# Optimization experiments

Measured on AMD Instinct MI355X. Metric: run time of the kernel, lower is better.

## Reference

```python
import jax, jax.numpy as jnp
import numpy as np

B, S, H, I, E, K = 4, 2048, 1024, 4096, 8, 2


def setup_inputs() -> dict:
    key = jax.random.key(0)
    ks = jax.random.split(key, 5)
    scale = 1.0 / np.sqrt(H)
    return {
        "hidden_states": jax.random.normal(ks[0], (B, S, H), dtype=jnp.float32),
        "router_w": jax.random.normal(ks[1], (E, H), dtype=jnp.float32) * scale,
        "gate_w": jax.random.normal(ks[2], (E, I, H), dtype=jnp.float32) * scale,
        "up_w": jax.random.normal(ks[3], (E, I, H), dtype=jnp.float32) * scale,
        "down_w": jax.random.normal(ks[4], (E, H, I), dtype=jnp.float32) * (1.0 / np.sqrt(I)),
        "top_k": K,
    }


def reference(hidden_states, router_w, gate_w, up_w, down_w, top_k):
    # Router: logits -> softmax -> top-k -> renormalized weights (eval mode, no jitter)
    logits = jnp.einsum("bsh,eh->bse", hidden_states, router_w)
    probs = jax.nn.softmax(logits, axis=-1)
    expert_weights, expert_indices = jax.lax.top_k(probs, top_k)  # [B,S,K]
    expert_weights = expert_weights / expert_weights.sum(axis=-1, keepdims=True)

    n_experts = router_w.shape[0]
    # Per-token combine weight for each expert: [B,S,E]
    combine = (jax.nn.one_hot(expert_indices, n_experts, dtype=expert_weights.dtype)
               * expert_weights[..., None]).sum(axis=-2)

    out = jnp.zeros_like(hidden_states)
    for e in range(n_experts):  # fixed small expert count
        g = jax.nn.silu(hidden_states @ gate_w[e].T)  # [B,S,I]
        u = hidden_states @ up_w[e].T                 # [B,S,I]
        y = (g * u) @ down_w[e].T                     # [B,S,H]
        out = out + combine[..., e:e + 1] * y
    return out
```

## Files before the change

### kernel.cpp

```cpp
#include <hip/hip_runtime.h>
#include <hip/hip_bf16.h>
#include <math.h>
#include <stdint.h>

#define TOKENS 8192
#define HD 1024
#define ID 4096
#define NE 8
#define RMAX 18432
#define MAXT 72

typedef __attribute__((ext_vector_type(8))) short short8v;
typedef __attribute__((ext_vector_type(4))) float f32x4;

typedef const __attribute__((address_space(1))) unsigned int* gas_u32p;
typedef __attribute__((address_space(3))) unsigned int* las_u32p;

__device__ __forceinline__ void stage16(const void* g, void* l) {
  __builtin_amdgcn_global_load_lds((gas_u32p)g, (las_u32p)l, 16, 0, 0);
}

#define BARRIER asm volatile("s_barrier" ::: "memory")
#define WAITLGKM asm volatile("s_waitcnt lgkmcnt(0)" ::: "memory")
#define VMC0 asm volatile("s_waitcnt vmcnt(0)" ::: "memory")
#define VMC3 asm volatile("s_waitcnt vmcnt(3)" ::: "memory")
#define VMC6 asm volatile("s_waitcnt vmcnt(6)" ::: "memory")

__global__ __launch_bounds__(256) void convert_kernel(const float* __restrict__ src,
                                                      __hip_bfloat16* __restrict__ dst) {
  size_t i = ((size_t)blockIdx.x * 256 + threadIdx.x) * 8;
  float4 a = ((const float4*)(src + i))[0];
  float4 b = ((const float4*)(src + i))[1];
  union { __hip_bfloat16 h[8]; int4 v; } u;
  u.h[0] = __float2bfloat16(a.x); u.h[1] = __float2bfloat16(a.y);
  u.h[2] = __float2bfloat16(a.z); u.h[3] = __float2bfloat16(a.w);
  u.h[4] = __float2bfloat16(b.x); u.h[5] = __float2bfloat16(b.y);
  u.h[6] = __float2bfloat16(b.z); u.h[7] = __float2bfloat16(b.w);
  *(int4*)(dst + i) = u.v;
}

__global__ __launch_bounds__(256) void router_kernel(
    const float* __restrict__ h, const float* __restrict__ rw,
    __hip_bfloat16* __restrict__ hx, int* __restrict__ tidx,
    float* __restrict__ tw, int* __restrict__ cnt) {
  int wid = threadIdx.x >> 6, lane = threadIdx.x & 63;
  int t = blockIdx.x * 4 + wid;
  const float4* h4 = (const float4*)(h + (size_t)t * HD);
  float x[16];
  {
    float4 xa = h4[lane * 4 + 0], xb = h4[lane * 4 + 1], xc = h4[lane * 4 + 2], xd = h4[lane * 4 + 3];
    x[0] = xa.x; x[1] = xa.y; x[2] = xa.z; x[3] = xa.w;
    x[4] = xb.x; x[5] = xb.y; x[6] = xb.z; x[7] = xb.w;
    x[8] = xc.x; x[9] = xc.y; x[10] = xc.z; x[11] = xc.w;
    x[12] = xd.x; x[13] = xd.y; x[14] = xd.z; x[15] = xd.w;
  }
  union { __hip_bfloat16 hb[16]; int4 v[2]; } u;
#pragma unroll
  for (int j = 0; j < 16; j++) u.hb[j] = __float2bfloat16(x[j]);
  {
    int4* hxp = (int4*)(hx + (size_t)t * HD + lane * 16);
    hxp[0] = u.v[0]; hxp[1] = u.v[1];
  }
  double acc[NE];
#pragma unroll
  for (int e = 0; e < NE; e++) {
    const float4* w4 = (const float4*)(rw + e * HD);
    float4 wa = w4[lane * 4 + 0], wb = w4[lane * 4 + 1], wc = w4[lane * 4 + 2], wd = w4[lane * 4 + 3];
    double s = 0.0;
    s += (double)x[0] * wa.x + (double)x[1] * wa.y + (double)x[2] * wa.z + (double)x[3] * wa.w;
    s += (double)x[4] * wb.x + (double)x[5] * wb.y + (double)x[6] * wb.z + (double)x[7] * wb.w;
    s += (double)x[8] * wc.x + (double)x[9] * wc.y + (double)x[10] * wc.z + (double)x[11] * wc.w;
    s += (double)x[12] * wd.x + (double)x[13] * wd.y + (double)x[14] * wd.z + (double)x[15] * wd.w;
    acc[e] = s;
  }
#pragma unroll
  for (int off = 32; off >= 1; off >>= 1)
#pragma unroll
    for (int e = 0; e < NE; e++) acc[e] += __shfl_xor(acc[e], off, 64);
  if (lane == 0) {
    int i0 = 0; double l0 = acc[0];
#pragma unroll
    for (int e = 1; e < NE; e++) if (acc[e] > l0) { l0 = acc[e]; i0 = e; }
    int i1 = -1; double l1 = -1.0e300;
#pragma unroll
    for (int e = 0; e < NE; e++) if (e != i0 && acc[e] > l1) { l1 = acc[e]; i1 = e; }
    double r = exp(l1 - l0);
    float w0 = (float)(1.0 / (1.0 + r));
    float w1 = (float)(r / (1.0 + r));
    tidx[t * 2 + 0] = i0; tidx[t * 2 + 1] = i1;
    tw[t * 2 + 0] = w0;  tw[t * 2 + 1] = w1;
    atomicAdd(&cnt[i0], 1); atomicAdd(&cnt[i1], 1);
  }
}

__global__ void scan_kernel(const int* __restrict__ cnt, int* __restrict__ ofs, int* __restrict__ cnt2) {
  if (threadIdx.x == 0) {
    int a = 0;
    for (int e = 0; e < NE; e++) { ofs[e] = a; a += (cnt[e] + 255) & ~255; }
    ofs[NE] = a;
  }
  if (threadIdx.x < NE) cnt2[threadIdx.x] = 0;
}

__global__ __launch_bounds__(256) void scatter_kernel(
    const int* __restrict__ tidx, const float* __restrict__ tw,
    const int* __restrict__ ofs, int* __restrict__ cnt2,
    int* __restrict__ rowmap, int* __restrict__ slots) {
  int t = blockIdx.x * 256 + threadIdx.x;
#pragma unroll
  for (int k = 0; k < 2; k++) {
    int e = tidx[t * 2 + k];
    int pos = atomicAdd(&cnt2[e], 1);
    int row = ofs[e] + pos;
    rowmap[row] = t;
    slots[t * 2 + k] = row;
  }
}

#define MFMAQ(ACC, MO, NO, AF, BF)                                                         \
  { _Pragma("unroll") for (int m_ = 0; m_ < 4; m_++)                                       \
    _Pragma("unroll") for (int n_ = 0; n_ < 2; n_++)                                       \
    _Pragma("unroll") for (int k_ = 0; k_ < 2; k_++)                                       \
      ACC[(MO) + m_][(NO) + n_] = __builtin_amdgcn_mfma_f32_16x16x32_bf16(                 \
          AF[m_][k_], BF[n_][k_], ACC[(MO) + m_][(NO) + n_], 0, 0, 0); }

__global__ __launch_bounds__(512, 2) void gemm1_kernel(
    const __hip_bfloat16* __restrict__ hx, const __hip_bfloat16* __restrict__ Wg,
    const __hip_bfloat16* __restrict__ Wu, const int* __restrict__ rowmap,
    const int* __restrict__ ofs, const __hip_bfloat16* __restrict__ zrow,
    __hip_bfloat16* __restrict__ act) {
  __shared__ __align__(128) char lds[131072];
  const int nwg = gridDim.x;
  int wg0 = blockIdx.x;
  int wg = (wg0 & 7) * (nwg >> 3) + (wg0 >> 3);
  const int tm = wg >> 5, tn = wg & 31;
  const int Rtot = ofs[NE];
  const int row0 = tm * 256;
  if (row0 >= Rtot) return;
  int e = 0;
#pragma unroll
  for (int i = 1; i < NE; i++) e += (row0 >= ofs[i]);
  const int tid = threadIdx.x, wid = tid >> 6, lane = tid & 63;
  const int wm = wid >> 1, wn = wid & 1;
  const int fr = lane & 15, fkE = (lane >> 4) << 3;
  const int wmB = wm * 64, wnB = wn * 64;

  const char* srcA[4]; const char* srcG[2]; const char* srcU[2];
  int ldA[4], ldG[2], ldU[2];
#pragma unroll
  for (int j = 0; j < 4; j++) {
    int d = j * 8192 + tid * 16;
    int row = d >> 7;
    int kb = (d ^ (((d >> 7) & 7) << 4)) & 127;
    int tok = rowmap[row0 + row];
    const __hip_bfloat16* base = (tok >= 0) ? (hx + (size_t)tok * HD) : zrow;
    srcA[j] = (const char*)base + kb;
    ldA[j] = j * 8192 + wid * 1024;
  }
#pragma unroll
  for (int j = 0; j < 2; j++) {
    int d = j * 8192 + tid * 16;
    int row = d >> 7;
    int kb = (d ^ (((d >> 7) & 7) << 4)) & 127;
    srcG[j] = (const char*)(Wg + ((size_t)e * ID + tn * 128 + row) * HD) + kb;
    srcU[j] = (const char*)(Wu + ((size_t)e * ID + tn * 128 + row) * HD) + kb;
    ldG[j] = 32768 + j * 8192 + wid * 1024;
    ldU[j] = 49152 + j * 8192 + wid * 1024;
  }
#define STG_A(j, t, bf) stage16(srcA[j] + (size_t)(t) * 128, (char*)lds + (bf) * 65536 + ldA[j])
#define STG_G(j, t, bf) stage16(srcG[j] + (size_t)(t) * 128, (char*)lds + (bf) * 65536 + ldG[j])
#define STG_U(j, t, bf) stage16(srcU[j] + (size_t)(t) * 128, (char*)lds + (bf) * 65536 + ldU[j])

  auto RD = [&](int bf, int poff, int rowi, int kki) -> short8v {
    int o = ((rowi + fr) << 7) + ((kki << 5) + fkE) * 2;
    o ^= ((o >> 7) & 7) << 4;
    return *(const short8v*)(&lds[bf * 65536 + poff + o]);
  };

  f32x4 accG[4][4], accU[4][4];
#pragma unroll
  for (int m = 0; m < 4; m++)
#pragma unroll
    for (int n = 0; n < 4; n++) { accG[m][n] = (f32x4)(0.0f); accU[m][n] = (f32x4)(0.0f); }

  const int NT = HD / 64;
#pragma unroll
  for (int j = 0; j < 4; j++) STG_A(j, 0, 0);
#pragma unroll
  for (int j = 0; j < 2; j++) STG_G(j, 0, 0);
#pragma unroll
  for (int j = 0; j < 2; j++) STG_U(j, 0, 0);
#pragma unroll
  for (int j = 0; j < 4; j++) STG_A(j, 1, 1);
#pragma unroll
  for (int j = 0; j < 2; j++) STG_G(j, 1, 1);
  VMC6; BARRIER;

#pragma unroll 1
  for (int I = 0; I < NT / 2; ++I) {
    const int t0 = 2 * I;
    const bool more = (t0 + 2 < NT);
    short8v a[4][2], bA[2][2], bB[2][2];
#pragma unroll
    for (int m = 0; m < 4; m++) { a[m][0] = RD(0, 0, wmB + m * 16, 0); a[m][1] = RD(0, 0, wmB + m * 16, 1); }
#pragma unroll
    for (int n = 0; n < 2; n++) { bA[n][0] = RD(0, 32768, wnB + n * 16, 0); bA[n][1] = RD(0, 32768, wnB + n * 16, 1); }
    STG_U(0, t0 + 1, 1); STG_U(1, t0 + 1, 1);
    BARRIER; WAITLGKM;
    __builtin_amdgcn_s_setprio(1); MFMAQ(accG, 0, 0, a, bA); __builtin_amdgcn_s_setprio(0);
    BARRIER;
#pragma unroll
    for (int n = 0; n < 2; n++) { bB[n][0] = RD(0, 32768, wnB + 32 + n * 16, 0); bB[n][1] = RD(0, 32768, wnB + 32 + n * 16, 1); }
    if (more) { STG_A(0, t0 + 2, 0); STG_A(1, t0 + 2, 0); }
    BARRIER; WAITLGKM;
    __builtin_amdgcn_s_setprio(1); MFMAQ(accG, 0, 2, a, bB); __builtin_amdgcn_s_setprio(0);
    BARRIER;
#pragma unroll
    for (int n = 0; n < 2; n++) { bA[n][0] = RD(0, 49152, wnB + n * 16, 0); bA[n][1] = RD(0, 49152, wnB + n * 16, 1); }
    if (more) { STG_A(2, t0 + 2, 0); STG_A(3, t0 + 2, 0); }
    BARRIER; WAITLGKM;
    __builtin_amdgcn_s_setprio(1); MFMAQ(accU, 0, 0, a, bA); __builtin_amdgcn_s_setprio(0);
    BARRIER;
#pragma unroll
    for (int n = 0; n < 2; n++) { bB[n][0] = RD(0, 49152, wnB + 32 + n * 16, 0); bB[n][1] = RD(0, 49152, wnB + 32 + n * 16, 1); }
    if (more) { STG_G(0, t0 + 2, 0); STG_G(1, t0 + 2, 0); }
    BARRIER; WAITLGKM;
    __builtin_amdgcn_s_setprio(1); MFMAQ(accU, 0, 2, a, bB); __builtin_amdgcn_s_setprio(0);
    if (more) { VMC6; } else { VMC0; }
    BARRIER;
#pragma unroll
    for (int m = 0; m < 4; m++) { a[m][0] = RD(1, 0, wmB + m * 16, 0); a[m][1] = RD(1, 0, wmB + m * 16, 1); }
#pragma unroll
    for (int n = 0; n < 2; n++) { bA[n][0] = RD(1, 32768, wnB + n * 16, 0); bA[n][1] = RD(1, 32768, wnB + n * 16, 1); }
    if (more) { STG_U(0, t0 + 2, 0); STG_U(1, t0 + 2, 0); }
    BARRIER; WAITLGKM;
    __builtin_amdgcn_s_setprio(1); MFMAQ(accG, 0, 0, a, bA); __builtin_amdgcn_s_setprio(0);
    BARRIER;
#pragma unroll
    for (int n = 0; n < 2; n++) { bB[n][0] = RD(1, 32768, wnB + 32 + n * 16, 0); bB[n][1] = RD(1, 32768, wnB + 32 + n * 16, 1); }
    if (more) { STG_A(0, t0 + 3, 1); STG_A(1, t0 + 3, 1); }
    BARRIER; WAITLGKM;
    __builtin_amdgcn_s_setprio(1); MFMAQ(accG, 0, 2, a, bB); __builtin_amdgcn_s_setprio(0);
    BARRIER;
#pragma unroll
    for (int n = 0; n < 2; n++) { bA[n][0] = RD(1, 49152, wnB + n * 16, 0); bA[n][1] = RD(1, 49152, wnB + n * 16, 1); }
    if (more) { STG_A(2, t0 + 3, 1); STG_A(3, t0 + 3, 1); }
    BARRIER; WAITLGKM;
    __builtin_amdgcn_s_setprio(1); MFMAQ(accU, 0, 0, a, bA); __builtin_amdgcn_s_setprio(0);
    BARRIER;
#pragma unroll
    for (int n = 0; n < 2; n++) { bB[n][0] = RD(1, 49152, wnB + 32 + n * 16, 0); bB[n][1] = RD(1, 49152, wnB + 32 + n * 16, 1); }
    if (more) { STG_G(0, t0 + 3, 1); STG_G(1, t0 + 3, 1); }
    BARRIER; WAITLGKM;
    __builtin_amdgcn_s_setprio(1); MFMAQ(accU, 0, 2, a, bB); __builtin_amdgcn_s_setprio(0);
    if (more) { VMC6; } else { VMC0; }
    BARRIER;
  }
#undef STG_A
#undef STG_G
#undef STG_U

  const int rb = row0 + wmB + ((lane >> 4) << 2);
  const int cb = tn * 128 + wnB + fr;
#pragma unroll
  for (int m = 0; m < 4; m++)
#pragma unroll
    for (int i = 0; i < 4; i++) {
      int r = rb + m * 16 + i;
      __hip_bfloat16* dst = act + (size_t)r * ID + cb;
#pragma unroll
      for (int n = 0; n < 4; n++) {
        float g = accG[m][n][i], uu = accU[m][n][i];
        float s = g / (1.0f + __expf(-g));
        dst[n * 16] = __float2bfloat16(s * uu);
      }
    }
}

__global__ __launch_bounds__(512, 2) void gemm2_kernel(
    const __hip_bfloat16* __restrict__ act, const __hip_bfloat16* __restrict__ Wd,
    const int* __restrict__ ofs, float* __restrict__ ybuf) {
  __shared__ __align__(128) char lds[98304];
  const int nwg = gridDim.x;
  int wg0 = blockIdx.x;
  int wg = (wg0 & 7) * (nwg >> 3) + (wg0 >> 3);
  const int tm = wg >> 3, tn = wg & 7;
  const int Rtot = ofs[NE];
  const int row0 = tm * 256;
  if (row0 >= Rtot) return;
  int e = 0;
#pragma unroll
  for (int i = 1; i < NE; i++) e += (row0 >= ofs[i]);
  const int tid = threadIdx.x, wid = tid >> 6, lane = tid & 63;
  const int wm = wid >> 1, wn = wid & 1;
  const int fr = lane & 15, fkE = (lane >> 4) << 3;
  const int wmB = wm * 64, wnB = wn * 64;

  const char* srcA[4]; const char* srcB[2];
  int ldA[4], ldB[2];
#pragma unroll
  for (int j = 0; j < 4; j++) {
    int d = j * 8192 + tid * 16;
    int row = d >> 7;
    int kb = (d ^ (((d >> 7) & 7) << 4)) & 127;
    srcA[j] = (const char*)(act + (size_t)(row0 + row) * ID) + kb;
    ldA[j] = j * 8192 + wid * 1024;
  }
#pragma unroll
  for (int j = 0; j < 2; j++) {
    int d = j * 8192 + tid * 16;
    int row = d >> 7;
    int kb = (d ^ (((d >> 7) & 7) << 4)) & 127;
    srcB[j] = (const char*)(Wd + ((size_t)e * HD + tn * 128 + row) * ID) + kb;
    ldB[j] = 32768 + j * 8192 + wid * 1024;
  }
#define STG_A2(j, t, bf) stage16(srcA[j] + (size_t)(t) * 128, (char*)lds + (bf) * 49152 + ldA[j])
#define STG_B2(j, t, bf) stage16(srcB[j] + (size_t)(t) * 128, (char*)lds + (bf) * 49152 + ldB[j])

  auto RD = [&](int bf, int poff, int rowi, int kki) -> short8v {
    int o = ((rowi + fr) << 7) + ((kki << 5) + fkE) * 2;
    o ^= ((o >> 7) & 7) << 4;
    return *(const short8v*)(&lds[bf * 49152 + poff + o]);
  };

  f32x4 acc[4][4];
#pragma unroll
  for (int m = 0; m < 4; m++)
#pragma unroll
    for (int n = 0; n < 4; n++) acc[m][n] = (f32x4)(0.0f);

  const int NT = ID / 64;
#pragma unroll
  for (int j = 0; j < 4; j++) STG_A2(j, 0, 0);
  STG_B2(0, 0, 0); STG_B2(1, 0, 0);
  STG_A2(0, 1, 1); STG_A2(1, 1, 1); STG_A2(2, 1, 1);
  VMC3; BARRIER;

#pragma unroll 1
  for (int I = 0; I < NT / 2; ++I) {
    const int T = 2 * I;
    const bool more = (T + 2 < NT);
    short8v a[4][2], b0[2][2], b1[2][2];
#pragma unroll
    for (int m = 0; m < 4; m++) { a[m][0] = RD(0, 0, wmB + m * 16, 0); a[m][1] = RD(0, 0, wmB + m * 16, 1); }
#pragma unroll
    for (int n = 0; n < 2; n++) { b0[n][0] = RD(0, 32768, wnB + n * 16, 0); b0[n][1] = RD(0, 32768, wnB + n * 16, 1); }
    STG_A2(3, T + 1, 1); STG_B2(0, T + 1, 1); STG_B2(1, T + 1, 1);
    BARRIER; WAITLGKM;
    __builtin_amdgcn_s_setprio(1); MFMAQ(acc, 0, 0, a, b0); __builtin_amdgcn_s_setprio(0);
    BARRIER;
#pragma unroll
    for (int n = 0; n < 2; n++) { b1[n][0] = RD(0, 32768, wnB + 32 + n * 16, 0); b1[n][1] = RD(0, 32768, wnB + 32 + n * 16, 1); }
    if (more) { STG_A2(0, T + 2, 0); STG_A2(1, T + 2, 0); STG_A2(2, T + 2, 0); }
    BARRIER; WAITLGKM;
    __builtin_amdgcn_s_setprio(1); MFMAQ(acc, 0, 2, a, b1); __builtin_amdgcn_s_setprio(0);
    if (more) { VMC3; } else { VMC0; }
    BARRIER;
#pragma unroll
    for (int m = 0; m < 4; m++) { a[m][0] = RD(1, 0, wmB + m * 16, 0); a[m][1] = RD(1, 0, wmB + m * 16, 1); }
#pragma unroll
    for (int n = 0; n < 2; n++) { b0[n][0] = RD(1, 32768, wnB + n * 16, 0); b0[n][1] = RD(1, 32768, wnB + n * 16, 1); }
    if (more) { STG_A2(3, T + 2, 0); STG_B2(0, T + 2, 0); STG_B2(1, T + 2, 0); }
    BARRIER; WAITLGKM;
    __builtin_amdgcn_s_setprio(1); MFMAQ(acc, 0, 0, a, b0); __builtin_amdgcn_s_setprio(0);
    BARRIER;
#pragma unroll
    for (int n = 0; n < 2; n++) { b1[n][0] = RD(1, 32768, wnB + 32 + n * 16, 0); b1[n][1] = RD(1, 32768, wnB + 32 + n * 16, 1); }
    if (more) { STG_A2(0, T + 3, 1); STG_A2(1, T + 3, 1); STG_A2(2, T + 3, 1); }
    BARRIER; WAITLGKM;
    __builtin_amdgcn_s_setprio(1); MFMAQ(acc, 0, 2, a, b1); __builtin_amdgcn_s_setprio(0);
    if (more) { VMC3; } else { VMC0; }
    BARRIER;
  }
#undef STG_A2
#undef STG_B2

  const int rb = row0 + wmB + ((lane >> 4) << 2);
  const int cb = tn * 128 + wnB + fr;
#pragma unroll
  for (int m = 0; m < 4; m++)
#pragma unroll
    for (int i = 0; i < 4; i++) {
      int r = rb + m * 16 + i;
      float* dst = ybuf + (size_t)r * HD + cb;
#pragma unroll
      for (int n = 0; n < 4; n++) dst[n * 16] = acc[m][n][i];
    }
}

__global__ __launch_bounds__(256) void combine_kernel(
    const float* __restrict__ ybuf, const int* __restrict__ slots,
    const float* __restrict__ tw, float* __restrict__ out) {
  int t = blockIdx.x * 4 + (threadIdx.x >> 6);
  int lane = threadIdx.x & 63;
  int r0 = slots[t * 2 + 0], r1 = slots[t * 2 + 1];
  float w0 = tw[t * 2 + 0], w1 = tw[t * 2 + 1];
  const float4* y0 = (const float4*)(ybuf + (size_t)r0 * HD);
  const float4* y1 = (const float4*)(ybuf + (size_t)r1 * HD);
  float4* o = (float4*)(out + (size_t)t * HD);
#pragma unroll
  for (int j = 0; j < 4; j++) {
    int ix = j * 64 + lane;
    float4 a = y0[ix], b = y1[ix];
    float4 c;
    c.x = w0 * a.x + w1 * b.x; c.y = w0 * a.y + w1 * b.y;
    c.z = w0 * a.z + w1 * b.z; c.w = w0 * a.w + w1 * b.w;
    o[ix] = c;
  }
}

extern "C" void kernel_launch(void* const* d_in, const int* in_sizes, int n_in,
                              void* d_out, int out_size, void* d_ws, size_t ws_size,
                              hipStream_t stream) {
  (void)in_sizes; (void)n_in; (void)out_size; (void)ws_size;
  const float* h  = (const float*)d_in[0];
  const float* rw = (const float*)d_in[1];
  const float* gw = (const float*)d_in[2];
  const float* uw = (const float*)d_in[3];
  const float* dw = (const float*)d_in[4];
  float* out = (float*)d_out;

  char* ws = (char*)d_ws;
  size_t off = 0;
  auto alloc = [&](size_t bytes) { char* p = ws + off; off += (bytes + 255) & ~255ULL; return p; };
  __hip_bfloat16* wg  = (__hip_bfloat16*)alloc((size_t)NE * ID * HD * 2);
  __hip_bfloat16* wu  = (__hip_bfloat16*)alloc((size_t)NE * ID * HD * 2);
  __hip_bfloat16* wd  = (__hip_bfloat16*)alloc((size_t)NE * HD * ID * 2);
  __hip_bfloat16* act = (__hip_bfloat16*)alloc((size_t)RMAX * ID * 2);
  __hip_bfloat16* hx  = (__hip_bfloat16*)alloc((size_t)TOKENS * HD * 2);
  float* ybuf = (float*)alloc((size_t)RMAX * HD * 4);
  __hip_bfloat16* zrow = (__hip_bfloat16*)alloc(HD * 2);
  int* rowmap = (int*)alloc(RMAX * 4);
  int* tidx   = (int*)alloc(TOKENS * 2 * 4);
  float* twt  = (float*)alloc(TOKENS * 2 * 4);
  int* slots  = (int*)alloc(TOKENS * 2 * 4);
  int* cnt    = (int*)alloc(256);
  int* cnt2   = (int*)alloc(256);
  int* ofs    = (int*)alloc(256);

  hipMemsetAsync(cnt, 0, NE * 4, stream);
  hipMemsetAsync(rowmap, 0xFF, RMAX * 4, stream);
  hipMemsetAsync(zrow, 0, HD * 2, stream);

  convert_kernel<<<16384, 256, 0, stream>>>(gw, wg);
  convert_kernel<<<16384, 256, 0, stream>>>(uw, wu);
  convert_kernel<<<16384, 256, 0, stream>>>(dw, wd);
  router_kernel<<<TOKENS / 4, 256, 0, stream>>>(h, rw, hx, tidx, twt, cnt);
  scan_kernel<<<1, 64, 0, stream>>>(cnt, ofs, cnt2);
  scatter_kernel<<<TOKENS / 256, 256, 0, stream>>>(tidx, twt, ofs, cnt2, rowmap, slots);
  gemm1_kernel<<<MAXT * 32, 512, 0, stream>>>(hx, wg, wu, rowmap, ofs, zrow, act);
  gemm2_kernel<<<MAXT * 8, 512, 0, stream>>>(act, wd, ofs, ybuf);
  combine_kernel<<<TOKENS / 4, 256, 0, stream>>>(ybuf, slots, twt, out);
}
```

Before: 898.1 us.

## Widen MFMA phases, triple-buffer gemm2 LDS, and fuse weight conversions into one launch

gemm1 now computes a full 4x4 MFMA block per phase instead of two half phases, which halves the barriers and LDS-read phases per K tile, and it issues each tile's staging loads in bigger batches with new vmcnt thresholds. gemm2 moves from a double-buffered, half-split loop to a three-stage LDS ring (144 KB) that prefetches two tiles ahead, with one barrier pair per K tile. The three fp32-to-bf16 weight conversions become a single launch that assumes the bf16 weight buffers sit back to back in memory. The aim is less synchronisation overhead and better overlap of loads with MFMA work, at the cost of much larger LDS use and more registers held live.

```diff
diff --git a/kernel.cpp b/kernel.cpp
--- a/kernel.cpp
+++ b/kernel.cpp
@@ -23,12 +23,17 @@
 #define BARRIER asm volatile("s_barrier" ::: "memory")
 #define WAITLGKM asm volatile("s_waitcnt lgkmcnt(0)" ::: "memory")
 #define VMC0 asm volatile("s_waitcnt vmcnt(0)" ::: "memory")
-#define VMC3 asm volatile("s_waitcnt vmcnt(3)" ::: "memory")
+#define VMC2 asm volatile("s_waitcnt vmcnt(2)" ::: "memory")
 #define VMC6 asm volatile("s_waitcnt vmcnt(6)" ::: "memory")
-
-__global__ __launch_bounds__(256) void convert_kernel(const float* __restrict__ src,
-                                                      __hip_bfloat16* __restrict__ dst) {
-  size_t i = ((size_t)blockIdx.x * 256 + threadIdx.x) * 8;
+#define VMC8 asm volatile("s_waitcnt vmcnt(8)" ::: "memory")
+
+__global__ __launch_bounds__(256) void convert3_kernel(
+    const float* __restrict__ s0, const float* __restrict__ s1, const float* __restrict__ s2,
+    __hip_bfloat16* __restrict__ d0) {
+  int r = blockIdx.x >> 14;
+  const float* src = (r == 0) ? s0 : ((r == 1) ? s1 : s2);
+  __hip_bfloat16* dst = d0 + (size_t)r * ((size_t)NE * ID * HD);
+  size_t i = (((size_t)(blockIdx.x & 16383)) * 256 + threadIdx.x) * 8;
   float4 a = ((const float4*)(src + i))[0];
   float4 b = ((const float4*)(src + i))[1];
   union { __hip_bfloat16 h[8]; int4 v; } u;
@@ -117,12 +122,12 @@
   }
 }
 
-#define MFMAQ(ACC, MO, NO, AF, BF)                                                         \
+#define MFMA44(ACC, AF, BF)                                                                \
   { _Pragma("unroll") for (int m_ = 0; m_ < 4; m_++)                                       \
-    _Pragma("unroll") for (int n_ = 0; n_ < 2; n_++)                                       \
+    _Pragma("unroll") for (int n_ = 0; n_ < 4; n_++)                                       \
     _Pragma("unroll") for (int k_ = 0; k_ < 2; k_++)                                       \
-      ACC[(MO) + m_][(NO) + n_] = __builtin_amdgcn_mfma_f32_16x16x32_bf16(                 \
-          AF[m_][k_], BF[n_][k_], ACC[(MO) + m_][(NO) + n_], 0, 0, 0); }
+      ACC[m_][n_] = __builtin_amdgcn_mfma_f32_16x16x32_bf16(                               \
+          AF[m_][k_], BF[n_][k_], ACC[m_][n_], 0, 0, 0); }
 
 __global__ __launch_bounds__(512, 2) void gemm1_kernel(
     const __hip_bfloat16* __restrict__ hx, const __hip_bfloat16* __restrict__ Wg,
@@ -186,74 +191,54 @@
   const int NT = HD / 64;
 #pragma unroll
   for (int j = 0; j < 4; j++) STG_A(j, 0, 0);
-#pragma unroll
-  for (int j = 0; j < 2; j++) STG_G(j, 0, 0);
-#pragma unroll
-  for (int j = 0; j < 2; j++) STG_U(j, 0, 0);
+  STG_G(0, 0, 0); STG_G(1, 0, 0);
+  STG_U(0, 0, 0); STG_U(1, 0, 0);
 #pragma unroll
   for (int j = 0; j < 4; j++) STG_A(j, 1, 1);
-#pragma unroll
-  for (int j = 0; j < 2; j++) STG_G(j, 1, 1);
-  VMC6; BARRIER;
+  STG_G(0, 1, 1); STG_G(1, 1, 1);
+  VMC8; BARRIER;
 
 #pragma unroll 1
   for (int I = 0; I < NT / 2; ++I) {
     const int t0 = 2 * I;
     const bool more = (t0 + 2 < NT);
-    short8v a[4][2], bA[2][2], bB[2][2];
+    short8v a[4][2], b[4][2];
 #pragma unroll
     for (int m = 0; m < 4; m++) { a[m][0] = RD(0, 0, wmB + m * 16, 0); a[m][1] = RD(0, 0, wmB + m * 16, 1); }
 #pragma unroll
-    for (int n = 0; n < 2; n++) { bA[n][0] = RD(0, 32768, wnB + n * 16, 0); bA[n][1] = RD(0, 32768, wnB + n * 16, 1); }
+    for (int n = 0; n < 4; n++) { b[n][0] = RD(0, 32768, wnB + n * 16, 0); b[n][1] = RD(0, 32768, wnB + n * 16, 1); }
     STG_U(0, t0 + 1, 1); STG_U(1, t0 + 1, 1);
     BARRIER; WAITLGKM;
-    __builtin_amdgcn_s_setprio(1); MFMAQ(accG, 0, 0, a, bA); __builtin_amdgcn_s_setprio(0);
+    __builtin_amdgcn_s_setprio(1); MFMA44(accG, a, b); __builtin_amdgcn_s_setprio(0);
+    VMC8; BARRIER;
+#pragma unroll
+    for (int n = 0; n < 4; n++) { b[n][0] = RD(0, 49152, wnB + n * 16, 0); b[n][1] = RD(0, 49152, wnB + n * 16, 1); }
+    if (more) {
+      STG_A(0, t0 + 2, 0); STG_A(1, t0 + 2, 0); STG_A(2, t0 + 2, 0); STG_A(3, t0 + 2, 0);
+      STG_G(0, t0 + 2, 0); STG_G(1, t0 + 2, 0);
+    }
+    BARRIER; WAITLGKM;
+    __builtin_amdgcn_s_setprio(1); MFMA44(accU, a, b); __builtin_amdgcn_s_setprio(0);
+    if (more) { VMC8; } else { VMC2; }
     BARRIER;
 #pragma unroll
-    for (int n = 0; n < 2; n++) { bB[n][0] = RD(0, 32768, wnB + 32 + n * 16, 0); bB[n][1] = RD(0, 32768, wnB + 32 + n * 16, 1); }
-    if (more) { STG_A(0, t0 + 2, 0); STG_A(1, t0 + 2, 0); }
-    BARRIER; WAITLGKM;
-    __builtin_amdgcn_s_setprio(1); MFMAQ(accG, 0, 2, a, bB); __builtin_amdgcn_s_setprio(0);
-    BARRIER;
-#pragma unroll
-    for (int n = 0; n < 2; n++) { bA[n][0] = RD(0, 49152, wnB + n * 16, 0); bA[n][1] = RD(0, 49152, wnB + n * 16, 1); }
-    if (more) { STG_A(2, t0 + 2, 0); STG_A(3, t0 + 2, 0); }
-    BARRIER; WAITLGKM;
-    __builtin_amdgcn_s_setprio(1); MFMAQ(accU, 0, 0, a, bA); __builtin_amdgcn_s_setprio(0);
-    BARRIER;
-#pragma unroll
-    for (int n = 0; n < 2; n++) { bB[n][0] = RD(0, 49152, wnB + 32 + n * 16, 0); bB[n][1] = RD(0, 49152, wnB + 32 + n * 16, 1); }
-    if (more) { STG_G(0, t0 + 2, 0); STG_G(1, t0 + 2, 0); }
-    BARRIER; WAITLGKM;
-    __builtin_amdgcn_s_setprio(1); MFMAQ(accU, 0, 2, a, bB); __builtin_amdgcn_s_setprio(0);
-    if (more) { VMC6; } else { VMC0; }
-    BARRIER;
-#pragma unroll
     for (int m = 0; m < 4; m++) { a[m][0] = RD(1, 0, wmB + m * 16, 0); a[m][1] = RD(1, 0, wmB + m * 16, 1); }
 #pragma unroll
-    for (int n = 0; n < 2; n++) { bA[n][0] = RD(1, 32768, wnB + n * 16, 0); bA[n][1] = RD(1, 32768, wnB + n * 16, 1); }
+    for (int n = 0; n < 4; n++) { b[n][0] = RD(1, 32768, wnB + n * 16, 0); b[n][1] = RD(1, 32768, wnB + n * 16, 1); }
     if (more) { STG_U(0, t0 + 2, 0); STG_U(1, t0 + 2, 0); }
     BARRIER; WAITLGKM;
-    __builtin_amdgcn_s_setprio(1); MFMAQ(accG, 0, 0, a, bA); __builtin_amdgcn_s_setprio(0);
+    __builtin_amdgcn_s_setprio(1); MFMA44(accG, a, b); __builtin_amdgcn_s_setprio(0);
+    if (more) { VMC8; } else { VMC0; }
     BARRIER;
 #pragma unroll
-    for (int n = 0; n < 2; n++) { bB[n][0] = RD(1, 32768, wnB + 32 + n * 16, 0); bB[n][1] = RD(1, 32768, wnB + 32 + n * 16, 1); }
-    if (more) { STG_A(0, t0 + 3, 1); STG_A(1, t0 + 3, 1); }
+    for (int n = 0; n < 4; n++) { b[n][0] = RD(1, 49152, wnB + n * 16, 0); b[n][1] = RD(1, 49152, wnB + n * 16, 1); }
+    if (more) {
+      STG_A(0, t0 + 3, 1); STG_A(1, t0 + 3, 1); STG_A(2, t0 + 3, 1); STG_A(3, t0 + 3, 1);
+      STG_G(0, t0 + 3, 1); STG_G(1, t0 + 3, 1);
+    }
     BARRIER; WAITLGKM;
-    __builtin_amdgcn_s_setprio(1); MFMAQ(accG, 0, 2, a, bB); __builtin_amdgcn_s_setprio(0);
-    BARRIER;
-#pragma unroll
-    for (int n = 0; n < 2; n++) { bA[n][0] = RD(1, 49152, wnB + n * 16, 0); bA[n][1] = RD(1, 49152, wnB + n * 16, 1); }
-    if (more) { STG_A(2, t0 + 3, 1); STG_A(3, t0 + 3, 1); }
-    BARRIER; WAITLGKM;
-    __builtin_amdgcn_s_setprio(1); MFMAQ(accU, 0, 0, a, bA); __builtin_amdgcn_s_setprio(0);
-    BARRIER;
-#pragma unroll
-    for (int n = 0; n < 2; n++) { bB[n][0] = RD(1, 49152, wnB + 32 + n * 16, 0); bB[n][1] = RD(1, 49152, wnB + 32 + n * 16, 1); }
-    if (more) { STG_G(0, t0 + 3, 1); STG_G(1, t0 + 3, 1); }
-    BARRIER; WAITLGKM;
-    __builtin_amdgcn_s_setprio(1); MFMAQ(accU, 0, 2, a, bB); __builtin_amdgcn_s_setprio(0);
-    if (more) { VMC6; } else { VMC0; }
+    __builtin_amdgcn_s_setprio(1); MFMA44(accU, a, b); __builtin_amdgcn_s_setprio(0);
+    if (more) { VMC8; } else { VMC0; }
     BARRIER;
   }
 #undef STG_A
@@ -280,7 +265,7 @@
 __global__ __launch_bounds__(512, 2) void gemm2_kernel(
     const __hip_bfloat16* __restrict__ act, const __hip_bfloat16* __restrict__ Wd,
     const int* __restrict__ ofs, float* __restrict__ ybuf) {
-  __shared__ __align__(128) char lds[98304];
+  __shared__ __align__(128) char lds[147456];
   const int nwg = gridDim.x;
   int wg0 = blockIdx.x;
   int wg = (wg0 & 7) * (nwg >> 3) + (wg0 >> 3);
@@ -314,13 +299,13 @@
     srcB[j] = (const char*)(Wd + ((size_t)e * HD + tn * 128 + row) * ID) + kb;
     ldB[j] = 32768 + j * 8192 + wid * 1024;
   }
-#define STG_A2(j, t, bf) stage16(srcA[j] + (size_t)(t) * 128, (char*)lds + (bf) * 49152 + ldA[j])
-#define STG_B2(j, t, bf) stage16(srcB[j] + (size_t)(t) * 128, (char*)lds + (bf) * 49152 + ldB[j])
-
-  auto RD = [&](int bf, int poff, int rowi, int kki) -> short8v {
+#define STG_A2(j, t, q) stage16(srcA[j] + (size_t)(t) * 128, (char*)lds + (q) * 49152 + ldA[j])
+#define STG_B2(j, t, q) stage16(srcB[j] + (size_t)(t) * 128, (char*)lds + (q) * 49152 + ldB[j])
+
+  auto RD = [&](const char* base, int poff, int rowi, int kki) -> short8v {
     int o = ((rowi + fr) << 7) + ((kki << 5) + fkE) * 2;
     o ^= ((o >> 7) & 7) << 4;
-    return *(const short8v*)(&lds[bf * 49152 + poff + o]);
+    return *(const short8v*)(base + poff + o);
   };
 
   f32x4 acc[4][4];
@@ -333,44 +318,31 @@
 #pragma unroll
   for (int j = 0; j < 4; j++) STG_A2(j, 0, 0);
   STG_B2(0, 0, 0); STG_B2(1, 0, 0);
-  STG_A2(0, 1, 1); STG_A2(1, 1, 1); STG_A2(2, 1, 1);
-  VMC3; BARRIER;
-
+#pragma unroll
+  for (int j = 0; j < 4; j++) STG_A2(j, 1, 1);
+  STG_B2(0, 1, 1); STG_B2(1, 1, 1);
+  VMC6; BARRIER;
+
+  int bq = 0;
 #pragma unroll 1
-  for (int I = 0; I < NT / 2; ++I) {
-    const int T = 2 * I;
+  for (int T = 0; T < NT; ++T) {
     const bool more = (T + 2 < NT);
-    short8v a[4][2], b0[2][2], b1[2][2];
-#pragma unroll
-    for (int m = 0; m < 4; m++) { a[m][0] = RD(0, 0, wmB + m * 16, 0); a[m][1] = RD(0, 0, wmB + m * 16, 1); }
-#pragma unroll
-    for (int n = 0; n < 2; n++) { b0[n][0] = RD(0, 32768, wnB + n * 16, 0); b0[n][1] = RD(0, 32768, wnB + n * 16, 1); }
-    STG_A2(3, T + 1, 1); STG_B2(0, T + 1, 1); STG_B2(1, T + 1, 1);
+    int sq = (bq >= 1) ? (bq - 1) : 2;
+    const char* base = (const char*)lds + bq * 49152;
+    short8v a[4][2], b[4][2];
+#pragma unroll
+    for (int m = 0; m < 4; m++) { a[m][0] = RD(base, 0, wmB + m * 16, 0); a[m][1] = RD(base, 0, wmB + m * 16, 1); }
+#pragma unroll
+    for (int n = 0; n < 4; n++) { b[n][0] = RD(base, 32768, wnB + n * 16, 0); b[n][1] = RD(base, 32768, wnB + n * 16, 1); }
+    if (more) {
+      STG_A2(0, T + 2, sq); STG_A2(1, T + 2, sq); STG_A2(2, T + 2, sq); STG_A2(3, T + 2, sq);
+      STG_B2(0, T + 2, sq); STG_B2(1, T + 2, sq);
+    }
     BARRIER; WAITLGKM;
-    __builtin_amdgcn_s_setprio(1); MFMAQ(acc, 0, 0, a, b0); __builtin_amdgcn_s_setprio(0);
+    __builtin_amdgcn_s_setprio(1); MFMA44(acc, a, b); __builtin_amdgcn_s_setprio(0);
+    if (more) { VMC6; } else { VMC0; }
     BARRIER;
-#pragma unroll
-    for (int n = 0; n < 2; n++) { b1[n][0] = RD(0, 32768, wnB + 32 + n * 16, 0); b1[n][1] = RD(0, 32768, wnB + 32 + n * 16, 1); }
-    if (more) { STG_A2(0, T + 2, 0); STG_A2(1, T + 2, 0); STG_A2(2, T + 2, 0); }
-    BARRIER; WAITLGKM;
-    __builtin_amdgcn_s_setprio(1); MFMAQ(acc, 0, 2, a, b1); __builtin_amdgcn_s_setprio(0);
-    if (more) { VMC3; } else { VMC0; }
-    BARRIER;
-#pragma unroll
-    for (int m = 0; m < 4; m++) { a[m][0] = RD(1, 0, wmB + m * 16, 0); a[m][1] = RD(1, 0, wmB + m * 16, 1); }
-#pragma unroll
-    for (int n = 0; n < 2; n++) { b0[n][0] = RD(1, 32768, wnB + n * 16, 0); b0[n][1] = RD(1, 32768, wnB + n * 16, 1); }
-    if (more) { STG_A2(3, T + 2, 0); STG_B2(0, T + 2, 0); STG_B2(1, T + 2, 0); }
-    BARRIER; WAITLGKM;
-    __builtin_amdgcn_s_setprio(1); MFMAQ(acc, 0, 0, a, b0); __builtin_amdgcn_s_setprio(0);
-    BARRIER;
-#pragma unroll
-    for (int n = 0; n < 2; n++) { b1[n][0] = RD(1, 32768, wnB + 32 + n * 16, 0); b1[n][1] = RD(1, 32768, wnB + 32 + n * 16, 1); }
-    if (more) { STG_A2(0, T + 3, 1); STG_A2(1, T + 3, 1); STG_A2(2, T + 3, 1); }
-    BARRIER; WAITLGKM;
-    __builtin_amdgcn_s_setprio(1); MFMAQ(acc, 0, 2, a, b1); __builtin_amdgcn_s_setprio(0);
-    if (more) { VMC3; } else { VMC0; }
-    BARRIER;
+    bq = (bq == 2) ? 0 : (bq + 1);
   }
 #undef STG_A2
 #undef STG_B2
@@ -442,9 +414,7 @@
   hipMemsetAsync(rowmap, 0xFF, RMAX * 4, stream);
   hipMemsetAsync(zrow, 0, HD * 2, stream);
 
-  convert_kernel<<<16384, 256, 0, stream>>>(gw, wg);
-  convert_kernel<<<16384, 256, 0, stream>>>(uw, wu);
-  convert_kernel<<<16384, 256, 0, stream>>>(dw, wd);
+  convert3_kernel<<<49152, 256, 0, stream>>>(gw, uw, dw, wg);
   router_kernel<<<TOKENS / 4, 256, 0, stream>>>(h, rw, hx, tidx, twt, cnt);
   scan_kernel<<<1, 64, 0, stream>>>(cnt, ofs, cnt2);
   scatter_kernel<<<TOKENS / 256, 256, 0, stream>>>(tidx, twt, ofs, cnt2, rowmap, slots);
```

Result: slower. 919.2 us (+2.3%).

## Fuse combine into gemm2 via atomic scatter and overlap down-weight conversion with gemm1

Applied to the files above, without the earlier changes.

Drops the fp32 ybuf intermediate and the combine kernel. gemm2 now scales each row by its routing weight and atomically adds it into the zeroed output at the owning token. The down-proj weight conversion moves into extra blocks of the gemm1 grid so it can overlap with GEMM work, and the gate/up conversions are merged into one launch. gemm1's tile order is remapped to row-major over MAXT. The cost is float atomics to global memory, which makes summation order nondeterministic, plus an extra memset of the output.

```diff
diff --git a/kernel.cpp b/kernel.cpp
--- a/kernel.cpp
+++ b/kernel.cpp
@@ -9,6 +9,8 @@
 #define NE 8
 #define RMAX 18432
 #define MAXT 72
+#define NG1 2304
+#define CVTD_BLOCKS 8192
 
 typedef __attribute__((ext_vector_type(8))) short short8v;
 typedef __attribute__((ext_vector_type(4))) float f32x4;
@@ -26,9 +28,13 @@
 #define VMC3 asm volatile("s_waitcnt vmcnt(3)" ::: "memory")
 #define VMC6 asm volatile("s_waitcnt vmcnt(6)" ::: "memory")
 
-__global__ __launch_bounds__(256) void convert_kernel(const float* __restrict__ src,
-                                                      __hip_bfloat16* __restrict__ dst) {
-  size_t i = ((size_t)blockIdx.x * 256 + threadIdx.x) * 8;
+__global__ __launch_bounds__(256) void convert_gu_kernel(
+    const float* __restrict__ s0, const float* __restrict__ s1,
+    __hip_bfloat16* __restrict__ d0) {
+  int r = blockIdx.x >> 14;
+  const float* src = (r == 0) ? s0 : s1;
+  __hip_bfloat16* dst = d0 + (size_t)r * ((size_t)NE * ID * HD);
+  size_t i = (((size_t)(blockIdx.x & 16383)) * 256 + threadIdx.x) * 8;
   float4 a = ((const float4*)(src + i))[0];
   float4 b = ((const float4*)(src + i))[1];
   union { __hip_bfloat16 h[8]; int4 v; } u;
@@ -105,7 +111,7 @@
 __global__ __launch_bounds__(256) void scatter_kernel(
     const int* __restrict__ tidx, const float* __restrict__ tw,
     const int* __restrict__ ofs, int* __restrict__ cnt2,
-    int* __restrict__ rowmap, int* __restrict__ slots) {
+    int* __restrict__ rowmap, float* __restrict__ wrow) {
   int t = blockIdx.x * 256 + threadIdx.x;
 #pragma unroll
   for (int k = 0; k < 2; k++) {
@@ -113,7 +119,7 @@
     int pos = atomicAdd(&cnt2[e], 1);
     int row = ofs[e] + pos;
     rowmap[row] = t;
-    slots[t * 2 + k] = row;
+    wrow[row] = tw[t * 2 + k];
   }
 }
 
@@ -128,19 +134,32 @@
     const __hip_bfloat16* __restrict__ hx, const __hip_bfloat16* __restrict__ Wg,
     const __hip_bfloat16* __restrict__ Wu, const int* __restrict__ rowmap,
     const int* __restrict__ ofs, const __hip_bfloat16* __restrict__ zrow,
-    __hip_bfloat16* __restrict__ act) {
+    __hip_bfloat16* __restrict__ act,
+    const float* __restrict__ dwsrc, __hip_bfloat16* __restrict__ wd) {
+  const int tid = threadIdx.x;
+  if (blockIdx.x >= NG1) {
+    size_t i = (((size_t)(blockIdx.x - NG1)) * 512 + tid) * 8;
+    float4 a = ((const float4*)(dwsrc + i))[0];
+    float4 b = ((const float4*)(dwsrc + i))[1];
+    union { __hip_bfloat16 h[8]; int4 v; } u;
+    u.h[0] = __float2bfloat16(a.x); u.h[1] = __float2bfloat16(a.y);
+    u.h[2] = __float2bfloat16(a.z); u.h[3] = __float2bfloat16(a.w);
+    u.h[4] = __float2bfloat16(b.x); u.h[5] = __float2bfloat16(b.y);
+    u.h[6] = __float2bfloat16(b.z); u.h[7] = __float2bfloat16(b.w);
+    *(int4*)(wd + i) = u.v;
+    return;
+  }
   __shared__ __align__(128) char lds[131072];
-  const int nwg = gridDim.x;
   int wg0 = blockIdx.x;
-  int wg = (wg0 & 7) * (nwg >> 3) + (wg0 >> 3);
-  const int tm = wg >> 5, tn = wg & 31;
+  int wg = (wg0 & 7) * (NG1 >> 3) + (wg0 >> 3);
+  const int tm = wg % MAXT, tn = wg / MAXT;
   const int Rtot = ofs[NE];
   const int row0 = tm * 256;
   if (row0 >= Rtot) return;
   int e = 0;
 #pragma unroll
   for (int i = 1; i < NE; i++) e += (row0 >= ofs[i]);
-  const int tid = threadIdx.x, wid = tid >> 6, lane = tid & 63;
+  const int wid = tid >> 6, lane = tid & 63;
   const int wm = wid >> 1, wn = wid & 1;
   const int fr = lane & 15, fkE = (lane >> 4) << 3;
   const int wmB = wm * 64, wnB = wn * 64;
@@ -279,7 +298,8 @@
 
 __global__ __launch_bounds__(512, 2) void gemm2_kernel(
     const __hip_bfloat16* __restrict__ act, const __hip_bfloat16* __restrict__ Wd,
-    const int* __restrict__ ofs, float* __restrict__ ybuf) {
+    const int* __restrict__ rowmap, const float* __restrict__ wrow,
+    const int* __restrict__ ofs, float* __restrict__ out) {
   __shared__ __align__(128) char lds[98304];
   const int nwg = gridDim.x;
   int wg0 = blockIdx.x;
@@ -375,44 +395,28 @@
 #undef STG_A2
 #undef STG_B2
 
-  const int rb = row0 + wmB + ((lane >> 4) << 2);
+  const int g4 = (lane >> 4) << 2;
   const int cb = tn * 128 + wnB + fr;
 #pragma unroll
-  for (int m = 0; m < 4; m++)
+  for (int m = 0; m < 4; m++) {
 #pragma unroll
     for (int i = 0; i < 4; i++) {
-      int r = rb + m * 16 + i;
-      float* dst = ybuf + (size_t)r * HD + cb;
-#pragma unroll
-      for (int n = 0; n < 4; n++) dst[n * 16] = acc[m][n][i];
+      int rr = row0 + wmB + m * 16 + g4 + i;
+      int tok = rowmap[rr];
+      if (tok >= 0) {
+        float w = wrow[rr];
+        float* dst = out + (size_t)tok * HD + cb;
+#pragma unroll
+        for (int n = 0; n < 4; n++) atomicAdd(dst + n * 16, w * acc[m][n][i]);
+      }
     }
-}
-
-__global__ __launch_bounds__(256) void combine_kernel(
-    const float* __restrict__ ybuf, const int* __restrict__ slots,
-    const float* __restrict__ tw, float* __restrict__ out) {
-  int t = blockIdx.x * 4 + (threadIdx.x >> 6);
-  int lane = threadIdx.x & 63;
-  int r0 = slots[t * 2 + 0], r1 = slots[t * 2 + 1];
-  float w0 = tw[t * 2 + 0], w1 = tw[t * 2 + 1];
-  const float4* y0 = (const float4*)(ybuf + (size_t)r0 * HD);
-  const float4* y1 = (const float4*)(ybuf + (size_t)r1 * HD);
-  float4* o = (float4*)(out + (size_t)t * HD);
-#pragma unroll
-  for (int j = 0; j < 4; j++) {
-    int ix = j * 64 + lane;
-    float4 a = y0[ix], b = y1[ix];
-    float4 c;
-    c.x = w0 * a.x + w1 * b.x; c.y = w0 * a.y + w1 * b.y;
-    c.z = w0 * a.z + w1 * b.z; c.w = w0 * a.w + w1 * b.w;
-    o[ix] = c;
   }
 }
 
 extern "C" void kernel_launch(void* const* d_in, const int* in_sizes, int n_in,
                               void* d_out, int out_size, void* d_ws, size_t ws_size,
                               hipStream_t stream) {
-  (void)in_sizes; (void)n_in; (void)out_size; (void)ws_size;
+  (void)in_sizes; (void)n_in; (void)ws_size;
   const float* h  = (const float*)d_in[0];
   const float* rw = (const float*)d_in[1];
   const float* gw = (const float*)d_in[2];
@@ -428,12 +432,11 @@
   __hip_bfloat16* wd  = (__hip_bfloat16*)alloc((size_t)NE * HD * ID * 2);
   __hip_bfloat16* act = (__hip_bfloat16*)alloc((size_t)RMAX * ID * 2);
   __hip_bfloat16* hx  = (__hip_bfloat16*)alloc((size_t)TOKENS * HD * 2);
-  float* ybuf = (float*)alloc((size_t)RMAX * HD * 4);
   __hip_bfloat16* zrow = (__hip_bfloat16*)alloc(HD * 2);
   int* rowmap = (int*)alloc(RMAX * 4);
+  float* wrow = (float*)alloc(RMAX * 4);
   int* tidx   = (int*)alloc(TOKENS * 2 * 4);
   float* twt  = (float*)alloc(TOKENS * 2 * 4);
-  int* slots  = (int*)alloc(TOKENS * 2 * 4);
   int* cnt    = (int*)alloc(256);
   int* cnt2   = (int*)alloc(256);
   int* ofs    = (int*)alloc(256);
@@ -441,14 +444,12 @@
   hipMemsetAsync(cnt, 0, NE * 4, stream);
   hipMemsetAsync(rowmap, 0xFF, RMAX * 4, stream);
   hipMemsetAsync(zrow, 0, HD * 2, stream);
-
-  convert_kernel<<<16384, 256, 0, stream>>>(gw, wg);
-  convert_kernel<<<16384, 256, 0, stream>>>(uw, wu);
-  convert_kernel<<<16384, 256, 0, stream>>>(dw, wd);
+  hipMemsetAsync(out, 0, (size_t)out_size * 4, stream);
+
+  convert_gu_kernel<<<32768, 256, 0, stream>>>(gw, uw, wg);
   router_kernel<<<TOKENS / 4, 256, 0, stream>>>(h, rw, hx, tidx, twt, cnt);
   scan_kernel<<<1, 64, 0, stream>>>(cnt, ofs, cnt2);
-  scatter_kernel<<<TOKENS / 256, 256, 0, stream>>>(tidx, twt, ofs, cnt2, rowmap, slots);
-  gemm1_kernel<<<MAXT * 32, 512, 0, stream>>>(hx, wg, wu, rowmap, ofs, zrow, act);
-  gemm2_kernel<<<MAXT * 8, 512, 0, stream>>>(act, wd, ofs, ybuf);
-  combine_kernel<<<TOKENS / 4, 256, 0, stream>>>(ybuf, slots, twt, out);
-}
+  scatter_kernel<<<TOKENS / 256, 256, 0, stream>>>(tidx, twt, ofs, cnt2, rowmap, wrow);
+  gemm1_kernel<<<NG1 + CVTD_BLOCKS, 512, 0, stream>>>(hx, wg, wu, rowmap, ofs, zrow, act, dw, wd);
+  gemm2_kernel<<<MAXT * 8, 512, 0, stream>>>(act, wd, rowmap, wrow, ofs, out);
+}
```

Measured after the change: 898.9 us. No clear change (+0.1%).
